# Kernel optimization log

Measured on AMD Instinct MI355X. Metric: run time of the kernel, lower is better.

The kernel has to match this reference:

```python
import jax, jax.numpy as jnp
import numpy as np

N = 50000   # nodes
E = 1600000 # edges (avg degree 32)
H = 128     # input_size == hidden_size
L = 2       # n_layer


def setup_inputs() -> dict:
    key = jax.random.key(0)
    k0, k1, k2, k3, k4 = jax.random.split(key, 5)
    inp = jax.random.normal(k0, (N, H), dtype=jnp.float32)
    h = jax.random.normal(k1, (L, N, H), dtype=jnp.float32)
    edgidx = jax.random.randint(k2, (2, E), 0, N, dtype=jnp.int32)
    # stacked gate linears, order per layer: xz, hz, xr, hr, xh, hh
    W = jax.random.normal(k3, (L, 6, H, H), dtype=jnp.float32) * (1.0 / np.sqrt(H))
    b = jax.random.normal(k4, (L, 6, H), dtype=jnp.float32) * 0.01
    return {"inp": inp, "edgidx": edgidx, "h": h, "W": W, "b": b}


def _gin(x, W, b, src, dst, n):
    # GINConv with eps=0: Linear(x + sum_{j in N(i)} x_j)
    agg = jax.ops.segment_sum(x[src], dst, num_segments=n)  # scatter-add over edges
    return (x + agg) @ W + b


def reference(inp, edgidx, h, W, b):
    src, dst = edgidx[0], edgidx[1]
    n = inp.shape[0]
    x = inp
    outs = []
    for i in range(W.shape[0]):  # small fixed layer loop
        z = jax.nn.sigmoid(_gin(x, W[i, 0], b[i, 0], src, dst, n)
                           + _gin(h[i], W[i, 1], b[i, 1], src, dst, n))
        r = jax.nn.sigmoid(_gin(x, W[i, 2], b[i, 2], src, dst, n)
                           + _gin(h[i], W[i, 3], b[i, 3], src, dst, n))
        h_tilde = jnp.tanh(_gin(x, W[i, 4], b[i, 4], src, dst, n)
                           + _gin(r * h[i], W[i, 5], b[i, 5], src, dst, n))
        x = z * h[i] + (1.0 - z) * h_tilde
        outs.append(x)
    h_out = jnp.stack(outs)  # [L, N, H]; original returns (out, h_out) where out is h_out
    return h_out
```

## Files before the change

### kernel.cpp

```cpp
#include <hip/hip_runtime.h>
#include <math.h>
#include <stdint.h>

#define HDIM 128

typedef _Float16 f16;
typedef unsigned short u16;
typedef __attribute__((ext_vector_type(8))) unsigned short u16x8;
typedef __attribute__((ext_vector_type(4))) _Float16 f16x4;
typedef __attribute__((ext_vector_type(8))) _Float16 f16x8;
typedef __attribute__((ext_vector_type(4))) float f32x4;

__global__ __launch_bounds__(256) void degrank_kernel(
    const int* __restrict__ edg, int* __restrict__ cnt,
    u16* __restrict__ rank, int E) {
  int e = blockIdx.x * 256 + threadIdx.x;
  if (e < E) {
    int src = edg[e];
    int dst = edg[E + e];
    rank[e] = (u16)atomicAdd(&cnt[dst * 16 + (src >> 12)], 1);
  }
}

__global__ __launch_bounds__(256) void nodescan_kernel(
    int* __restrict__ cnt, int* __restrict__ deg, int* __restrict__ degt,
    int N) {
  int node = blockIdx.x * 256 + threadIdx.x;
  if (node >= N) return;
  int* c = cnt + node * 16;
  int s = 0;
  #pragma unroll
  for (int b = 0; b < 16; ++b) {
    int v = c[b];
    c[b] = s;
    s += v;
  }
  degt[node] = s;
  deg[node] = (s + 7) & ~7;
}

__global__ __launch_bounds__(256) void scan_part_kernel(
    const int* __restrict__ deg, int* __restrict__ bsum, int n, int chunk) {
  __shared__ int red[256];
  const int b = blockIdx.x, t = threadIdx.x;
  const int begin = b * chunk;
  const int end = min(begin + chunk, n);
  int s = 0;
  for (int i = begin + t; i < end; i += 256) s += deg[i];
  red[t] = s;
  __syncthreads();
  for (int off = 128; off > 0; off >>= 1) {
    if (t < off) red[t] += red[t + off];
    __syncthreads();
  }
  if (t == 0) bsum[b] = red[0];
}

__global__ __launch_bounds__(256) void scan_top_kernel(
    const int* __restrict__ bsum, int* __restrict__ boff,
    int* __restrict__ offs, int n) {
  __shared__ int sh[256];
  const int t = threadIdx.x;
  int v = bsum[t];
  sh[t] = v;
  __syncthreads();
  for (int off = 1; off < 256; off <<= 1) {
    int add = (t >= off) ? sh[t - off] : 0;
    __syncthreads();
    sh[t] += add;
    __syncthreads();
  }
  boff[t] = sh[t] - v;
  if (t == 255) offs[n] = sh[255];
}

__global__ __launch_bounds__(256) void scan_fin_kernel(
    const int* __restrict__ deg, const int* __restrict__ boff,
    int* __restrict__ offs, int n, int chunk) {
  __shared__ int sh[256];
  const int b = blockIdx.x, t = threadIdx.x;
  const int idx = b * chunk + t;
  int v = (t < chunk && idx < n) ? deg[idx] : 0;
  sh[t] = v;
  __syncthreads();
  for (int off = 1; off < 256; off <<= 1) {
    int add = (t >= off) ? sh[t - off] : 0;
    __syncthreads();
    sh[t] += add;
    __syncthreads();
  }
  if (t < chunk && idx < n) offs[idx] = boff[b] + sh[t] - v;
}

__global__ __launch_bounds__(256) void fill_kernel(
    const int* __restrict__ edg, const int* __restrict__ offs,
    const int* __restrict__ cnt, const u16* __restrict__ rank,
    u16* __restrict__ csr_src, int E) {
  int i = blockIdx.x * 256 + threadIdx.x;
  int e0 = i * 4;
  if (e0 >= E) return;
  if (e0 + 4 <= E) {
    int4 s4 = *reinterpret_cast<const int4*>(edg + e0);
    int4 d4 = *reinterpret_cast<const int4*>(edg + E + e0);
    ushort4 r4 = *reinterpret_cast<const ushort4*>(rank + e0);
    csr_src[offs[d4.x] + cnt[d4.x * 16 + (s4.x >> 12)] + r4.x] = (u16)s4.x;
    csr_src[offs[d4.y] + cnt[d4.y * 16 + (s4.y >> 12)] + r4.y] = (u16)s4.y;
    csr_src[offs[d4.z] + cnt[d4.z * 16 + (s4.z >> 12)] + r4.z] = (u16)s4.z;
    csr_src[offs[d4.w] + cnt[d4.w * 16 + (s4.w >> 12)] + r4.w] = (u16)s4.w;
  } else {
    for (int e = e0; e < E; ++e) {
      int src = edg[e];
      int dst = edg[E + e];
      csr_src[offs[dst] + cnt[dst * 16 + (src >> 12)] + rank[e]] = (u16)src;
    }
  }
}

__global__ __launch_bounds__(256) void pad_kernel(
    const int* __restrict__ offs, const int* __restrict__ degt,
    const int* __restrict__ deg, u16* __restrict__ csr, int N) {
  int n = blockIdx.x * 256 + threadIdx.x;
  if (n >= N) return;
  int base = offs[n];
  int a = degt[n], b = deg[n];
  for (int k = base + a; k < base + b; ++k) csr[k] = (u16)N;
}

__global__ __launch_bounds__(256) void zpad_kernel(
    f16* __restrict__ xb, f16* __restrict__ cb, f16* __restrict__ hb,
    int N, int L) {
  int t = threadIdx.x;
  int rows = 2 + L;
  int total = 4 * rows * 4;
  if (t >= total) return;
  int chunk = t & 3;
  int r = (t >> 2) % rows;
  int sl = (t >> 2) / rows;
  size_t SN1 = (size_t)(N + 1);
  f16* p;
  if (r == 0)      p = xb + (sl * SN1 + N) * 32;
  else if (r == 1) p = cb + (sl * SN1 + N) * 32;
  else {
    int i = r - 2;
    p = hb + ((size_t)sl * L * SN1 + (size_t)i * SN1 + N) * 32;
  }
  f16x8 z{};
  *reinterpret_cast<f16x8*>(p + chunk * 8) = z;
}

__global__ __launch_bounds__(256) void convb_kernel(
    const float* __restrict__ src, f16* __restrict__ dst, int n, int SN,
    int rowoff) {
  const int t = threadIdx.x;
  const int nloc = t >> 3;
  const int sub = t & 7;
  const int sl = sub >> 1;
  const int hf = sub & 1;
  const int node = blockIdx.x * 32 + nloc;
  if (node >= n) return;
  const float* sp = src + (size_t)node * HDIM + sub * 16;
  f16* dp = dst + ((size_t)sl * SN + rowoff + node) * 32 + hf * 16;
  float4 v0 = *reinterpret_cast<const float4*>(sp + 0);
  float4 v1 = *reinterpret_cast<const float4*>(sp + 4);
  float4 v2 = *reinterpret_cast<const float4*>(sp + 8);
  float4 v3 = *reinterpret_cast<const float4*>(sp + 12);
  f16x8 o0, o1;
  o0[0]=(f16)v0.x; o0[1]=(f16)v0.y; o0[2]=(f16)v0.z; o0[3]=(f16)v0.w;
  o0[4]=(f16)v1.x; o0[5]=(f16)v1.y; o0[6]=(f16)v1.z; o0[7]=(f16)v1.w;
  o1[0]=(f16)v2.x; o1[1]=(f16)v2.y; o1[2]=(f16)v2.z; o1[3]=(f16)v2.w;
  o1[4]=(f16)v3.x; o1[5]=(f16)v3.y; o1[6]=(f16)v3.z; o1[7]=(f16)v3.w;
  *reinterpret_cast<f16x8*>(dp) = o0;
  *reinterpret_cast<f16x8*>(dp + 8) = o1;
}

__global__ __launch_bounds__(256) void transw_kernel(
    const float* __restrict__ W, f16* __restrict__ WT) {
  __shared__ float sh[32][33];
  const int g = blockIdx.y;
  const int ti = blockIdx.x >> 2;
  const int tj = blockIdx.x & 3;
  const float* __restrict__ wp = W + (size_t)g * HDIM * HDIM;
  f16* __restrict__ op = WT + (size_t)g * HDIM * HDIM;
  const int t = threadIdx.x;
  #pragma unroll
  for (int it = 0; it < 4; ++it) {
    int elem = it * 256 + t;
    int r = elem >> 5, c = elem & 31;
    sh[r][c] = wp[(size_t)(ti * 32 + r) * HDIM + tj * 32 + c];
  }
  __syncthreads();
  #pragma unroll
  for (int it = 0; it < 4; ++it) {
    int elem = it * 256 + t;
    int cc = elem >> 5, rr = elem & 31;
    op[(size_t)(tj * 32 + cc) * HDIM + ti * 32 + rr] = (f16)sh[rr][cc];
  }
}

__global__ __launch_bounds__(256) void pull2_kernel(
    const u16* __restrict__ csr_src, const int* __restrict__ offs,
    const f16* __restrict__ xb, const f16* __restrict__ hbl,
    f16* __restrict__ A, f16* __restrict__ Bh, int N, int N1, int hSN) {
  const int cls = blockIdx.x & 7;
  const int tid = cls >> 2;
  const int sl = cls & 3;
  const int node = (blockIdx.x >> 3) * 64 + (threadIdx.x >> 2);
  if (node >= N) return;
  const int c8 = (threadIdx.x & 3) << 3;
  const f16* __restrict__ tab =
      tid ? hbl + (size_t)sl * hSN * 32 : xb + (size_t)sl * (size_t)N1 * 32;
  f16* __restrict__ dst = (tid ? Bh : A) + (size_t)sl * (size_t)N1 * 32;
  const int s = offs[node];
  const int e = offs[node + 1];
  float acc[8];
  f16x8 sv = *reinterpret_cast<const f16x8*>(tab + (size_t)node * 32 + c8);
  #pragma unroll
  for (int q = 0; q < 8; ++q) acc[q] = (float)sv[q];
  int k = s;
  for (; k + 16 <= e; k += 16) {
    u16x8 ia = *reinterpret_cast<const u16x8*>(csr_src + k);
    u16x8 ib = *reinterpret_cast<const u16x8*>(csr_src + k + 8);
    f16x8 u0 = *reinterpret_cast<const f16x8*>(tab + (size_t)ia[0] * 32 + c8);
    f16x8 u1 = *reinterpret_cast<const f16x8*>(tab + (size_t)ia[1] * 32 + c8);
    f16x8 u2 = *reinterpret_cast<const f16x8*>(tab + (size_t)ia[2] * 32 + c8);
    f16x8 u3 = *reinterpret_cast<const f16x8*>(tab + (size_t)ia[3] * 32 + c8);
    f16x8 u4 = *reinterpret_cast<const f16x8*>(tab + (size_t)ia[4] * 32 + c8);
    f16x8 u5 = *reinterpret_cast<const f16x8*>(tab + (size_t)ia[5] * 32 + c8);
    f16x8 u6 = *reinterpret_cast<const f16x8*>(tab + (size_t)ia[6] * 32 + c8);
    f16x8 u7 = *reinterpret_cast<const f16x8*>(tab + (size_t)ia[7] * 32 + c8);
    f16x8 u8 = *reinterpret_cast<const f16x8*>(tab + (size_t)ib[0] * 32 + c8);
    f16x8 u9 = *reinterpret_cast<const f16x8*>(tab + (size_t)ib[1] * 32 + c8);
    f16x8 ua = *reinterpret_cast<const f16x8*>(tab + (size_t)ib[2] * 32 + c8);
    f16x8 ub = *reinterpret_cast<const f16x8*>(tab + (size_t)ib[3] * 32 + c8);
    f16x8 uc = *reinterpret_cast<const f16x8*>(tab + (size_t)ib[4] * 32 + c8);
    f16x8 ud = *reinterpret_cast<const f16x8*>(tab + (size_t)ib[5] * 32 + c8);
    f16x8 ue = *reinterpret_cast<const f16x8*>(tab + (size_t)ib[6] * 32 + c8);
    f16x8 uf = *reinterpret_cast<const f16x8*>(tab + (size_t)ib[7] * 32 + c8);
    f16x8 g0 = (u0 + u1) + (u2 + u3);
    f16x8 g1 = (u4 + u5) + (u6 + u7);
    f16x8 g2 = (u8 + u9) + (ua + ub);
    f16x8 g3 = (uc + ud) + (ue + uf);
    #pragma unroll
    for (int q = 0; q < 8; ++q)
      acc[q] += ((float)g0[q] + (float)g1[q]) + ((float)g2[q] + (float)g3[q]);
  }
  if (k < e) {
    u16x8 ia = *reinterpret_cast<const u16x8*>(csr_src + k);
    f16x8 u0 = *reinterpret_cast<const f16x8*>(tab + (size_t)ia[0] * 32 + c8);
    f16x8 u1 = *reinterpret_cast<const f16x8*>(tab + (size_t)ia[1] * 32 + c8);
    f16x8 u2 = *reinterpret_cast<const f16x8*>(tab + (size_t)ia[2] * 32 + c8);
    f16x8 u3 = *reinterpret_cast<const f16x8*>(tab + (size_t)ia[3] * 32 + c8);
    f16x8 u4 = *reinterpret_cast<const f16x8*>(tab + (size_t)ia[4] * 32 + c8);
    f16x8 u5 = *reinterpret_cast<const f16x8*>(tab + (size_t)ia[5] * 32 + c8);
    f16x8 u6 = *reinterpret_cast<const f16x8*>(tab + (size_t)ia[6] * 32 + c8);
    f16x8 u7 = *reinterpret_cast<const f16x8*>(tab + (size_t)ia[7] * 32 + c8);
    f16x8 g0 = (u0 + u1) + (u2 + u3);
    f16x8 g1 = (u4 + u5) + (u6 + u7);
    #pragma unroll
    for (int q = 0; q < 8; ++q) acc[q] += (float)g0[q] + (float)g1[q];
  }
  f16x8 o;
  #pragma unroll
  for (int q = 0; q < 8; ++q) o[q] = (f16)acc[q];
  *reinterpret_cast<f16x8*>(dst + (size_t)node * 32 + c8) = o;
}

__global__ __launch_bounds__(256) void pull1_kernel(
    const u16* __restrict__ csr_src, const int* __restrict__ offs,
    const f16* __restrict__ cb, f16* __restrict__ Ctot, int N, int N1) {
  const int sl = blockIdx.x & 3;
  const int node = (blockIdx.x >> 2) * 64 + (threadIdx.x >> 2);
  if (node >= N) return;
  const int c8 = (threadIdx.x & 3) << 3;
  const f16* __restrict__ tab = cb + (size_t)sl * (size_t)N1 * 32;
  f16* __restrict__ dst = Ctot + (size_t)sl * (size_t)N1 * 32;
  const int s = offs[node];
  const int e = offs[node + 1];
  float acc[8];
  f16x8 sv = *reinterpret_cast<const f16x8*>(tab + (size_t)node * 32 + c8);
  #pragma unroll
  for (int q = 0; q < 8; ++q) acc[q] = (float)sv[q];
  int k = s;
  for (; k + 16 <= e; k += 16) {
    u16x8 ia = *reinterpret_cast<const u16x8*>(csr_src + k);
    u16x8 ib = *reinterpret_cast<const u16x8*>(csr_src + k + 8);
    f16x8 u0 = *reinterpret_cast<const f16x8*>(tab + (size_t)ia[0] * 32 + c8);
    f16x8 u1 = *reinterpret_cast<const f16x8*>(tab + (size_t)ia[1] * 32 + c8);
    f16x8 u2 = *reinterpret_cast<const f16x8*>(tab + (size_t)ia[2] * 32 + c8);
    f16x8 u3 = *reinterpret_cast<const f16x8*>(tab + (size_t)ia[3] * 32 + c8);
    f16x8 u4 = *reinterpret_cast<const f16x8*>(tab + (size_t)ia[4] * 32 + c8);
    f16x8 u5 = *reinterpret_cast<const f16x8*>(tab + (size_t)ia[5] * 32 + c8);
    f16x8 u6 = *reinterpret_cast<const f16x8*>(tab + (size_t)ia[6] * 32 + c8);
    f16x8 u7 = *reinterpret_cast<const f16x8*>(tab + (size_t)ia[7] * 32 + c8);
    f16x8 u8 = *reinterpret_cast<const f16x8*>(tab + (size_t)ib[0] * 32 + c8);
    f16x8 u9 = *reinterpret_cast<const f16x8*>(tab + (size_t)ib[1] * 32 + c8);
    f16x8 ua = *reinterpret_cast<const f16x8*>(tab + (size_t)ib[2] * 32 + c8);
    f16x8 ub = *reinterpret_cast<const f16x8*>(tab + (size_t)ib[3] * 32 + c8);
    f16x8 uc = *reinterpret_cast<const f16x8*>(tab + (size_t)ib[4] * 32 + c8);
    f16x8 ud = *reinterpret_cast<const f16x8*>(tab + (size_t)ib[5] * 32 + c8);
    f16x8 ue = *reinterpret_cast<const f16x8*>(tab + (size_t)ib[6] * 32 + c8);
    f16x8 uf = *reinterpret_cast<const f16x8*>(tab + (size_t)ib[7] * 32 + c8);
    f16x8 g0 = (u0 + u1) + (u2 + u3);
    f16x8 g1 = (u4 + u5) + (u6 + u7);
    f16x8 g2 = (u8 + u9) + (ua + ub);
    f16x8 g3 = (uc + ud) + (ue + uf);
    #pragma unroll
    for (int q = 0; q < 8; ++q)
      acc[q] += ((float)g0[q] + (float)g1[q]) + ((float)g2[q] + (float)g3[q]);
  }
  if (k < e) {
    u16x8 ia = *reinterpret_cast<const u16x8*>(csr_src + k);
    f16x8 u0 = *reinterpret_cast<const f16x8*>(tab + (size_t)ia[0] * 32 + c8);
    f16x8 u1 = *reinterpret_cast<const f16x8*>(tab + (size_t)ia[1] * 32 + c8);
    f16x8 u2 = *reinterpret_cast<const f16x8*>(tab + (size_t)ia[2] * 32 + c8);
    f16x8 u3 = *reinterpret_cast<const f16x8*>(tab + (size_t)ia[3] * 32 + c8);
    f16x8 u4 = *reinterpret_cast<const f16x8*>(tab + (size_t)ia[4] * 32 + c8);
    f16x8 u5 = *reinterpret_cast<const f16x8*>(tab + (size_t)ia[5] * 32 + c8);
    f16x8 u6 = *reinterpret_cast<const f16x8*>(tab + (size_t)ia[6] * 32 + c8);
    f16x8 u7 = *reinterpret_cast<const f16x8*>(tab + (size_t)ia[7] * 32 + c8);
    f16x8 g0 = (u0 + u1) + (u2 + u3);
    f16x8 g1 = (u4 + u5) + (u6 + u7);
    #pragma unroll
    for (int q = 0; q < 8; ++q) acc[q] += (float)g0[q] + (float)g1[q];
  }
  f16x8 o;
  #pragma unroll
  for (int q = 0; q < 8; ++q) o[q] = (f16)acc[q];
  *reinterpret_cast<f16x8*>(dst + (size_t)node * 32 + c8) = o;
}

__device__ __forceinline__ void stage_blocked(
    const f16* __restrict__ src, f16* __restrict__ As,
    int row0, int N, int SN, int t) {
  #pragma unroll
  for (int i = 0; i < 4; ++i) {
    int u = i * 256 + t;
    int row = u >> 4;
    int sl = (u >> 2) & 3;
    int ck = u & 3;
    int r = row0 + row;
    f16x8 v{};
    if (r < N) v = *reinterpret_cast<const f16x8*>(
        src + ((size_t)sl * SN + r) * 32 + ck * 8);
    *reinterpret_cast<f16x8*>(&As[row * 136 + sl * 32 + ck * 8]) = v;
  }
}

__device__ __forceinline__ void mfma_tile(
    const f16* As, const f16* Ws, int wr, int wc, int ln15, int quad,
    f32x4 (&acc)[2][4]) {
  #pragma unroll
  for (int s = 0; s < 4; ++s) {
    f16x8 a0 = *reinterpret_cast<const f16x8*>(
        &As[(wr * 32 + ln15) * 136 + s * 32 + quad * 8]);
    f16x8 a1 = *reinterpret_cast<const f16x8*>(
        &As[(wr * 32 + 16 + ln15) * 136 + s * 32 + quad * 8]);
    #pragma unroll
    for (int ni = 0; ni < 4; ++ni) {
      f16x8 bf = *reinterpret_cast<const f16x8*>(
          &Ws[(wc * 64 + ni * 16 + ln15) * 136 + s * 32 + quad * 8]);
      acc[0][ni] = __builtin_amdgcn_mfma_f32_16x16x32_f16(a0, bf, acc[0][ni], 0, 0, 0);
      acc[1][ni] = __builtin_amdgcn_mfma_f32_16x16x32_f16(a1, bf, acc[1][ni], 0, 0, 0);
    }
  }
}

__global__ __launch_bounds__(256, 3) void gemm3_kernel(
    const f16* __restrict__ A, const f16* __restrict__ Bh,
    const f16* __restrict__ WT, const float* __restrict__ b,
    const f16* __restrict__ hbl, f16* __restrict__ zb,
    f16* __restrict__ cb, float* __restrict__ hpre, int N, int N1, int hSN) {
  __shared__ f16 As[64 * 136];
  __shared__ f16 Ws[128 * 136];
  const int t = threadIdx.x;
  const int w = t >> 6, wr = w >> 1, wc = w & 1;
  const int lane = t & 63, ln15 = lane & 15, quad = lane >> 4;
  const int row0 = blockIdx.x * 64;
  f32x4 accZ[2][4], accR[2][4], accH[2][4];
  #pragma unroll
  for (int i = 0; i < 2; ++i)
    #pragma unroll
    for (int j = 0; j < 4; ++j) {
      accZ[i][j] = (f32x4){0.f, 0.f, 0.f, 0.f};
      accR[i][j] = (f32x4){0.f, 0.f, 0.f, 0.f};
      accH[i][j] = (f32x4){0.f, 0.f, 0.f, 0.f};
    }

  stage_blocked(A, As, row0, N, N1, t);
  #pragma unroll
  for (int g = 0; g < 3; ++g) {
    const f16* __restrict__ wp = WT + (size_t)(g * 2) * HDIM * HDIM;
    __syncthreads();
    #pragma unroll
    for (int i = 0; i < 8; ++i) {
      int flat = i * 256 + t;
      int n = flat >> 4;
      int o = (flat & 15) * 8;
      *reinterpret_cast<f16x8*>(&Ws[n * 136 + o]) =
          *reinterpret_cast<const f16x8*>(wp + (size_t)n * HDIM + o);
    }
    __syncthreads();
    if (g == 0) mfma_tile(As, Ws, wr, wc, ln15, quad, accZ);
    else if (g == 1) mfma_tile(As, Ws, wr, wc, ln15, quad, accR);
    else mfma_tile(As, Ws, wr, wc, ln15, quad, accH);
  }
  __syncthreads();
  stage_blocked(Bh, As, row0, N, N1, t);
  #pragma unroll
  for (int g = 0; g < 2; ++g) {
    const f16* __restrict__ wp = WT + (size_t)(g * 2 + 1) * HDIM * HDIM;
    __syncthreads();
    #pragma unroll
    for (int i = 0; i < 8; ++i) {
      int flat = i * 256 + t;
      int n = flat >> 4;
      int o = (flat & 15) * 8;
      *reinterpret_cast<f16x8*>(&Ws[n * 136 + o]) =
          *reinterpret_cast<const f16x8*>(wp + (size_t)n * HDIM + o);
    }
    __syncthreads();
    if (g == 0) mfma_tile(As, Ws, wr, wc, ln15, quad, accZ);
    else mfma_tile(As, Ws, wr, wc, ln15, quad, accR);
  }

  #pragma unroll
  for (int ni = 0; ni < 4; ++ni) {
    const int col = wc * 64 + ni * 16 + ln15;
    const int slc = col >> 5;
    const int cw = col & 31;
    float bz = b[0 * HDIM + col] + b[1 * HDIM + col];
    float br = b[2 * HDIM + col] + b[3 * HDIM + col];
    float bh = b[4 * HDIM + col];
    #pragma unroll
    for (int mi = 0; mi < 2; ++mi) {
      #pragma unroll
      for (int r = 0; r < 4; ++r) {
        int row = row0 + wr * 32 + mi * 16 + quad * 4 + r;
        if (row >= N) continue;
        size_t idx = (size_t)row * HDIM + col;
        zb[idx] = (f16)(accZ[mi][ni][r] + bz);
        float rv = accR[mi][ni][r] + br;
        float rg = 1.f / (1.f + expf(-rv));
        float hv = (float)hbl[((size_t)slc * hSN + row) * 32 + cw];
        cb[((size_t)slc * N1 + row) * 32 + cw] = (f16)(rg * hv);
        hpre[idx] = accH[mi][ni][r] + bh;
      }
    }
  }
}

__global__ __launch_bounds__(256, 3) void gemm_final_kernel(
    const f16* __restrict__ Ctot, const f16* __restrict__ WT5,
    const float* __restrict__ b5, const f16* __restrict__ zb,
    const f16* __restrict__ hbl, float* __restrict__ outi,
    f16* __restrict__ xb, int N, int N1, int hSN) {
  __shared__ f16 As[64 * 136];
  __shared__ f16 Ws[128 * 136];
  const int t = threadIdx.x;
  const int w = t >> 6, wr = w >> 1, wc = w & 1;
  const int lane = t & 63, ln15 = lane & 15, quad = lane >> 4;
  const int row0 = blockIdx.x * 64;
  f32x4 acc[2][4];
  #pragma unroll
  for (int i = 0; i < 2; ++i)
    #pragma unroll
    for (int j = 0; j < 4; ++j) acc[i][j] = (f32x4){0.f, 0.f, 0.f, 0.f};

  stage_blocked(Ctot, As, row0, N, N1, t);
  #pragma unroll
  for (int i = 0; i < 8; ++i) {
    int flat = i * 256 + t;
    int n = flat >> 4;
    int o = (flat & 15) * 8;
    *reinterpret_cast<f16x8*>(&Ws[n * 136 + o]) =
        *reinterpret_cast<const f16x8*>(WT5 + (size_t)n * HDIM + o);
  }
  __syncthreads();
  mfma_tile(As, Ws, wr, wc, ln15, quad, acc);

  #pragma unroll
  for (int ni = 0; ni < 4; ++ni) {
    const int col = wc * 64 + ni * 16 + ln15;
    const int slc = col >> 5;
    const int cw = col & 31;
    float bias = b5[col];
    #pragma unroll
    for (int mi = 0; mi < 2; ++mi) {
      #pragma unroll
      for (int r = 0; r < 4; ++r) {
        int row = row0 + wr * 32 + mi * 16 + quad * 4 + r;
        if (row >= N) continue;
        size_t idx = (size_t)row * HDIM + col;
        float v = acc[mi][ni][r] + bias + outi[idx];
        float ht = tanhf(v);
        float z = 1.f / (1.f + expf(-(float)zb[idx]));
        float hv = (float)hbl[((size_t)slc * hSN + row) * 32 + cw];
        float o = z * hv + (1.f - z) * ht;
        outi[idx] = o;
        xb[((size_t)slc * N1 + row) * 32 + cw] = (f16)o;
      }
    }
  }
}

extern "C" void kernel_launch(void* const* d_in, const int* in_sizes, int n_in,
                              void* d_out, int out_size, void* d_ws, size_t ws_size,
                              hipStream_t stream) {
  const float* inp = (const float*)d_in[0];
  const int*   edg = (const int*)d_in[1];
  const float* h   = (const float*)d_in[2];
  const float* W   = (const float*)d_in[3];
  const float* b   = (const float*)d_in[4];
  float* out = (float*)d_out;

  const int NH = in_sizes[0];
  const int N  = NH / HDIM;
  const int E  = in_sizes[1] / 2;
  const int L  = in_sizes[2] / NH;
  const int N1 = N + 1;
  const size_t NT = (size_t)128 * N1;

  f16* Af   = (f16*)d_ws;
  f16* Bhf  = Af + NT;
  f16* cbuf = Bhf + NT;
  f16* xbuf = cbuf + NT;
  f16* hbuf = xbuf + NT;
  f16* zbuf = hbuf + (size_t)L * NT;
  f16* WT   = zbuf + (size_t)NH;
  int* deg     = (int*)(WT + (size_t)L * 6 * HDIM * HDIM);
  int* degt    = deg + N;
  int* offs    = degt + N;
  int* bsum    = offs + (N + 1);
  int* boff    = bsum + 256;
  uintptr_t rp = (uintptr_t)(boff + 256);
  rp = (rp + 63) & ~(uintptr_t)63;
  u16* rank    = (u16*)rp;
  u16* csr_src = rank + (size_t)E;
  int* cnt     = (int*)Af;

  const int eblocks = (E + 255) / 256;
  const int fblocks = (E + 1023) / 1024;
  const int nsblocks = (N + 255) / 256;
  const int rowblocks = (N + 63) / 64;
  const int p2blocks = ((N + 63) / 64) * 8;
  const int p1blocks = ((N + 63) / 64) * 4;
  const int cvblocks = (N + 31) / 32;
  const int chunk = (N + 255) / 256;
  const int hSN = L * N1;

  hipMemsetAsync(cnt, 0, (size_t)N * 16 * sizeof(int), stream);
  hipLaunchKernelGGL(degrank_kernel, dim3(eblocks), dim3(256), 0, stream,
                     edg, cnt, rank, E);
  hipLaunchKernelGGL(nodescan_kernel, dim3(nsblocks), dim3(256), 0, stream,
                     cnt, deg, degt, N);
  hipLaunchKernelGGL(scan_part_kernel, dim3(256), dim3(256), 0, stream,
                     deg, bsum, N, chunk);
  hipLaunchKernelGGL(scan_top_kernel, dim3(1), dim3(256), 0, stream,
                     bsum, boff, offs, N);
  hipLaunchKernelGGL(scan_fin_kernel, dim3(256), dim3(256), 0, stream,
                     deg, boff, offs, N, chunk);
  hipLaunchKernelGGL(fill_kernel, dim3(fblocks), dim3(256), 0, stream,
                     edg, offs, cnt, rank, csr_src, E);
  hipLaunchKernelGGL(pad_kernel, dim3(nsblocks), dim3(256), 0, stream,
                     offs, degt, deg, csr_src, N);
  hipLaunchKernelGGL(transw_kernel, dim3(16, L * 6), dim3(256), 0, stream,
                     W, WT);
  hipLaunchKernelGGL(convb_kernel, dim3(cvblocks), dim3(256), 0, stream,
                     inp, xbuf, N, N1, 0);
  for (int i = 0; i < L; ++i)
    hipLaunchKernelGGL(convb_kernel, dim3(cvblocks), dim3(256), 0, stream,
                       h + (size_t)i * NH, hbuf, N, hSN, i * N1);
  hipLaunchKernelGGL(zpad_kernel, dim3(1), dim3(256), 0, stream,
                     xbuf, cbuf, hbuf, N, L);

  for (int i = 0; i < L; ++i) {
    const f16* hbl = hbuf + (size_t)i * N1 * 32;
    const f16* WTi = WT + (size_t)i * 6 * HDIM * HDIM;
    const float* bi = b + (size_t)i * 6 * HDIM;
    float* outi = out + (size_t)i * NH;

    hipLaunchKernelGGL(pull2_kernel, dim3(p2blocks), dim3(256), 0, stream,
                       csr_src, offs, xbuf, hbl, Af, Bhf, N, N1, hSN);
    hipLaunchKernelGGL(gemm3_kernel, dim3(rowblocks), dim3(256), 0, stream,
                       Af, Bhf, WTi, bi, hbl, zbuf, cbuf, outi, N, N1, hSN);
    hipLaunchKernelGGL(pull1_kernel, dim3(p1blocks), dim3(256), 0, stream,
                       csr_src, offs, cbuf, Af, N, N1);
    hipLaunchKernelGGL(gemm_final_kernel, dim3(rowblocks), dim3(256), 0, stream,
                       Af, WTi + (size_t)5 * HDIM * HDIM, bi + 5 * HDIM,
                       zbuf, hbl, outi, xbuf, N, N1, hSN);
  }
}
```

Before: 667.2 us.

## Apply hh linear before aggregation and fuse final GRU step into pull kernel

Uses linearity of the GIN hh branch, (c + A c) W = c W + A (c W), so gemm3 now multiplies r*h by W_hh in-tile and writes the projected P. The final kernel aggregates P over neighbors and applies the tanh/GRU combine directly. This removes the separate gemm_final launch and its reload of the aggregated buffer and weights. It also merges the three conversion launches into one 2D grid and folds zero-padding into pad_kernel to cut launch count. The trade-off is extra work and shared memory traffic inside gemm3, plus aggregation of f16-rounded projected values instead of raw inputs.

```diff
diff --git a/kernel.cpp b/kernel.cpp
--- a/kernel.cpp
+++ b/kernel.cpp
@@ -118,39 +118,45 @@
 
 __global__ __launch_bounds__(256) void pad_kernel(
     const int* __restrict__ offs, const int* __restrict__ degt,
-    const int* __restrict__ deg, u16* __restrict__ csr, int N) {
+    const int* __restrict__ deg, u16* __restrict__ csr,
+    f16* __restrict__ xb, f16* __restrict__ Pb, f16* __restrict__ hb,
+    int N, int L) {
   int n = blockIdx.x * 256 + threadIdx.x;
-  if (n >= N) return;
-  int base = offs[n];
-  int a = degt[n], b = deg[n];
-  for (int k = base + a; k < base + b; ++k) csr[k] = (u16)N;
-}
-
-__global__ __launch_bounds__(256) void zpad_kernel(
-    f16* __restrict__ xb, f16* __restrict__ cb, f16* __restrict__ hb,
-    int N, int L) {
-  int t = threadIdx.x;
-  int rows = 2 + L;
-  int total = 4 * rows * 4;
-  if (t >= total) return;
-  int chunk = t & 3;
-  int r = (t >> 2) % rows;
-  int sl = (t >> 2) / rows;
-  size_t SN1 = (size_t)(N + 1);
-  f16* p;
-  if (r == 0)      p = xb + (sl * SN1 + N) * 32;
-  else if (r == 1) p = cb + (sl * SN1 + N) * 32;
-  else {
-    int i = r - 2;
-    p = hb + ((size_t)sl * L * SN1 + (size_t)i * SN1 + N) * 32;
-  }
-  f16x8 z{};
-  *reinterpret_cast<f16x8*>(p + chunk * 8) = z;
+  if (n < N) {
+    int base = offs[n];
+    int a = degt[n], b = deg[n];
+    for (int k = base + a; k < base + b; ++k) csr[k] = (u16)N;
+  } else {
+    int t2 = n - N;
+    int rows = 2 + L;
+    int total = 4 * rows * 4;
+    if (t2 < total) {
+      int chunk = t2 & 3;
+      int r = (t2 >> 2) % rows;
+      int sl = (t2 >> 2) / rows;
+      size_t SN1 = (size_t)(N + 1);
+      f16* p;
+      if (r == 0)      p = xb + (sl * SN1 + N) * 32;
+      else if (r == 1) p = Pb + (sl * SN1 + N) * 32;
+      else {
+        int i = r - 2;
+        p = hb + ((size_t)sl * L * SN1 + (size_t)i * SN1 + N) * 32;
+      }
+      f16x8 z{};
+      *reinterpret_cast<f16x8*>(p + chunk * 8) = z;
+    }
+  }
 }
 
 __global__ __launch_bounds__(256) void convb_kernel(
-    const float* __restrict__ src, f16* __restrict__ dst, int n, int SN,
-    int rowoff) {
+    const float* __restrict__ inp, const float* __restrict__ h,
+    f16* __restrict__ xb, f16* __restrict__ hb, int n, int N1, int NH,
+    int L) {
+  const int ly = blockIdx.y;
+  const float* __restrict__ src = (ly == 0) ? inp : h + (size_t)(ly - 1) * NH;
+  f16* __restrict__ dstb = (ly == 0) ? xb : hb;
+  const int SN = (ly == 0) ? N1 : L * N1;
+  const int rowoff = (ly == 0) ? 0 : (ly - 1) * N1;
   const int t = threadIdx.x;
   const int nloc = t >> 3;
   const int sub = t & 7;
@@ -159,7 +165,7 @@
   const int node = blockIdx.x * 32 + nloc;
   if (node >= n) return;
   const float* sp = src + (size_t)node * HDIM + sub * 16;
-  f16* dp = dst + ((size_t)sl * SN + rowoff + node) * 32 + hf * 16;
+  f16* dp = dstb + ((size_t)sl * SN + rowoff + node) * 32 + hf * 16;
   float4 v0 = *reinterpret_cast<const float4*>(sp + 0);
   float4 v1 = *reinterpret_cast<const float4*>(sp + 4);
   float4 v2 = *reinterpret_cast<const float4*>(sp + 8);
@@ -265,15 +271,174 @@
   *reinterpret_cast<f16x8*>(dst + (size_t)node * 32 + c8) = o;
 }
 
-__global__ __launch_bounds__(256) void pull1_kernel(
+__device__ __forceinline__ void stage_blocked(
+    const f16* __restrict__ src, f16* __restrict__ As,
+    int row0, int N, int SN, int t) {
+  #pragma unroll
+  for (int i = 0; i < 4; ++i) {
+    int u = i * 256 + t;
+    int row = u >> 4;
+    int sl = (u >> 2) & 3;
+    int ck = u & 3;
+    int r = row0 + row;
+    f16x8 v{};
+    if (r < N) v = *reinterpret_cast<const f16x8*>(
+        src + ((size_t)sl * SN + r) * 32 + ck * 8);
+    *reinterpret_cast<f16x8*>(&As[row * 136 + sl * 32 + ck * 8]) = v;
+  }
+}
+
+__device__ __forceinline__ void mfma_tile(
+    const f16* As, const f16* Ws, int wr, int wc, int ln15, int quad,
+    f32x4 (&acc)[2][4]) {
+  #pragma unroll
+  for (int s = 0; s < 4; ++s) {
+    f16x8 a0 = *reinterpret_cast<const f16x8*>(
+        &As[(wr * 32 + ln15) * 136 + s * 32 + quad * 8]);
+    f16x8 a1 = *reinterpret_cast<const f16x8*>(
+        &As[(wr * 32 + 16 + ln15) * 136 + s * 32 + quad * 8]);
+    #pragma unroll
+    for (int ni = 0; ni < 4; ++ni) {
+      f16x8 bf = *reinterpret_cast<const f16x8*>(
+          &Ws[(wc * 64 + ni * 16 + ln15) * 136 + s * 32 + quad * 8]);
+      acc[0][ni] = __builtin_amdgcn_mfma_f32_16x16x32_f16(a0, bf, acc[0][ni], 0, 0, 0);
+      acc[1][ni] = __builtin_amdgcn_mfma_f32_16x16x32_f16(a1, bf, acc[1][ni], 0, 0, 0);
+    }
+  }
+}
+
+__global__ __launch_bounds__(256, 3) void gemm3_kernel(
+    const f16* __restrict__ A, const f16* __restrict__ Bh,
+    const f16* __restrict__ WT, const float* __restrict__ b,
+    const f16* __restrict__ hbl, f16* __restrict__ zb,
+    f16* __restrict__ P, float* __restrict__ hpre, int N, int N1, int hSN) {
+  __shared__ f16 As[64 * 136];
+  __shared__ f16 Ws[128 * 136];
+  const int t = threadIdx.x;
+  const int w = t >> 6, wr = w >> 1, wc = w & 1;
+  const int lane = t & 63, ln15 = lane & 15, quad = lane >> 4;
+  const int row0 = blockIdx.x * 64;
+  f32x4 accZ[2][4], accR[2][4], accH[2][4];
+  #pragma unroll
+  for (int i = 0; i < 2; ++i)
+    #pragma unroll
+    for (int j = 0; j < 4; ++j) {
+      accZ[i][j] = (f32x4){0.f, 0.f, 0.f, 0.f};
+      accR[i][j] = (f32x4){0.f, 0.f, 0.f, 0.f};
+      accH[i][j] = (f32x4){0.f, 0.f, 0.f, 0.f};
+    }
+
+  stage_blocked(A, As, row0, N, N1, t);
+  #pragma unroll
+  for (int g = 0; g < 3; ++g) {
+    const f16* __restrict__ wp = WT + (size_t)(g * 2) * HDIM * HDIM;
+    __syncthreads();
+    #pragma unroll
+    for (int i = 0; i < 8; ++i) {
+      int flat = i * 256 + t;
+      int n = flat >> 4;
+      int o = (flat & 15) * 8;
+      *reinterpret_cast<f16x8*>(&Ws[n * 136 + o]) =
+          *reinterpret_cast<const f16x8*>(wp + (size_t)n * HDIM + o);
+    }
+    __syncthreads();
+    if (g == 0) mfma_tile(As, Ws, wr, wc, ln15, quad, accZ);
+    else if (g == 1) mfma_tile(As, Ws, wr, wc, ln15, quad, accR);
+    else mfma_tile(As, Ws, wr, wc, ln15, quad, accH);
+  }
+  __syncthreads();
+  stage_blocked(Bh, As, row0, N, N1, t);
+  #pragma unroll
+  for (int g = 0; g < 2; ++g) {
+    const f16* __restrict__ wp = WT + (size_t)(g * 2 + 1) * HDIM * HDIM;
+    __syncthreads();
+    #pragma unroll
+    for (int i = 0; i < 8; ++i) {
+      int flat = i * 256 + t;
+      int n = flat >> 4;
+      int o = (flat & 15) * 8;
+      *reinterpret_cast<f16x8*>(&Ws[n * 136 + o]) =
+          *reinterpret_cast<const f16x8*>(wp + (size_t)n * HDIM + o);
+    }
+    __syncthreads();
+    if (g == 0) mfma_tile(As, Ws, wr, wc, ln15, quad, accZ);
+    else mfma_tile(As, Ws, wr, wc, ln15, quad, accR);
+  }
+  __syncthreads();
+
+  {
+    const f16* __restrict__ wp = WT + (size_t)5 * HDIM * HDIM;
+    #pragma unroll
+    for (int i = 0; i < 8; ++i) {
+      int flat = i * 256 + t;
+      int n = flat >> 4;
+      int o = (flat & 15) * 8;
+      *reinterpret_cast<f16x8*>(&Ws[n * 136 + o]) =
+          *reinterpret_cast<const f16x8*>(wp + (size_t)n * HDIM + o);
+    }
+  }
+  #pragma unroll
+  for (int ni = 0; ni < 4; ++ni) {
+    const int col = wc * 64 + ni * 16 + ln15;
+    const int slc = col >> 5;
+    const int cw = col & 31;
+    float bz = b[0 * HDIM + col] + b[1 * HDIM + col];
+    float br = b[2 * HDIM + col] + b[3 * HDIM + col];
+    float bh = b[4 * HDIM + col] + b[5 * HDIM + col];
+    #pragma unroll
+    for (int mi = 0; mi < 2; ++mi) {
+      #pragma unroll
+      for (int r = 0; r < 4; ++r) {
+        int rowl = wr * 32 + mi * 16 + quad * 4 + r;
+        int row = row0 + rowl;
+        float rv = accR[mi][ni][r] + br;
+        float rg = 1.f / (1.f + expf(-rv));
+        float hv = 0.f;
+        if (row < N) {
+          size_t idx = (size_t)row * HDIM + col;
+          zb[idx] = (f16)(accZ[mi][ni][r] + bz);
+          hpre[idx] = accH[mi][ni][r] + bh;
+          hv = (float)hbl[((size_t)slc * hSN + row) * 32 + cw];
+        }
+        As[rowl * 136 + col] = (f16)(rg * hv);
+      }
+    }
+  }
+  __syncthreads();
+  f32x4 accP[2][4];
+  #pragma unroll
+  for (int i = 0; i < 2; ++i)
+    #pragma unroll
+    for (int j = 0; j < 4; ++j) accP[i][j] = (f32x4){0.f, 0.f, 0.f, 0.f};
+  mfma_tile(As, Ws, wr, wc, ln15, quad, accP);
+
+  #pragma unroll
+  for (int ni = 0; ni < 4; ++ni) {
+    const int col = wc * 64 + ni * 16 + ln15;
+    const int slc = col >> 5;
+    const int cw = col & 31;
+    #pragma unroll
+    for (int mi = 0; mi < 2; ++mi) {
+      #pragma unroll
+      for (int r = 0; r < 4; ++r) {
+        int row = row0 + wr * 32 + mi * 16 + quad * 4 + r;
+        if (row >= N) continue;
+        P[((size_t)slc * N1 + row) * 32 + cw] = (f16)accP[mi][ni][r];
+      }
+    }
+  }
+}
+
+__global__ __launch_bounds__(256) void gru_final_kernel(
     const u16* __restrict__ csr_src, const int* __restrict__ offs,
-    const f16* __restrict__ cb, f16* __restrict__ Ctot, int N, int N1) {
+    const f16* __restrict__ P, const f16* __restrict__ zb,
+    const f16* __restrict__ hbl, float* __restrict__ outi,
+    f16* __restrict__ xb, int N, int N1, int hSN) {
   const int sl = blockIdx.x & 3;
   const int node = (blockIdx.x >> 2) * 64 + (threadIdx.x >> 2);
   if (node >= N) return;
   const int c8 = (threadIdx.x & 3) << 3;
-  const f16* __restrict__ tab = cb + (size_t)sl * (size_t)N1 * 32;
-  f16* __restrict__ dst = Ctot + (size_t)sl * (size_t)N1 * 32;
+  const f16* __restrict__ tab = P + (size_t)sl * (size_t)N1 * 32;
   const int s = offs[node];
   const int e = offs[node + 1];
   float acc[8];
@@ -323,184 +488,26 @@
     #pragma unroll
     for (int q = 0; q < 8; ++q) acc[q] += (float)g0[q] + (float)g1[q];
   }
-  f16x8 o;
-  #pragma unroll
-  for (int q = 0; q < 8; ++q) o[q] = (f16)acc[q];
-  *reinterpret_cast<f16x8*>(dst + (size_t)node * 32 + c8) = o;
-}
-
-__device__ __forceinline__ void stage_blocked(
-    const f16* __restrict__ src, f16* __restrict__ As,
-    int row0, int N, int SN, int t) {
-  #pragma unroll
-  for (int i = 0; i < 4; ++i) {
-    int u = i * 256 + t;
-    int row = u >> 4;
-    int sl = (u >> 2) & 3;
-    int ck = u & 3;
-    int r = row0 + row;
-    f16x8 v{};
-    if (r < N) v = *reinterpret_cast<const f16x8*>(
-        src + ((size_t)sl * SN + r) * 32 + ck * 8);
-    *reinterpret_cast<f16x8*>(&As[row * 136 + sl * 32 + ck * 8]) = v;
-  }
-}
-
-__device__ __forceinline__ void mfma_tile(
-    const f16* As, const f16* Ws, int wr, int wc, int ln15, int quad,
-    f32x4 (&acc)[2][4]) {
-  #pragma unroll
-  for (int s = 0; s < 4; ++s) {
-    f16x8 a0 = *reinterpret_cast<const f16x8*>(
-        &As[(wr * 32 + ln15) * 136 + s * 32 + quad * 8]);
-    f16x8 a1 = *reinterpret_cast<const f16x8*>(
-        &As[(wr * 32 + 16 + ln15) * 136 + s * 32 + quad * 8]);
-    #pragma unroll
-    for (int ni = 0; ni < 4; ++ni) {
-      f16x8 bf = *reinterpret_cast<const f16x8*>(
-          &Ws[(wc * 64 + ni * 16 + ln15) * 136 + s * 32 + quad * 8]);
-      acc[0][ni] = __builtin_amdgcn_mfma_f32_16x16x32_f16(a0, bf, acc[0][ni], 0, 0, 0);
-      acc[1][ni] = __builtin_amdgcn_mfma_f32_16x16x32_f16(a1, bf, acc[1][ni], 0, 0, 0);
-    }
-  }
-}
-
-__global__ __launch_bounds__(256, 3) void gemm3_kernel(
-    const f16* __restrict__ A, const f16* __restrict__ Bh,
-    const f16* __restrict__ WT, const float* __restrict__ b,
-    const f16* __restrict__ hbl, f16* __restrict__ zb,
-    f16* __restrict__ cb, float* __restrict__ hpre, int N, int N1, int hSN) {
-  __shared__ f16 As[64 * 136];
-  __shared__ f16 Ws[128 * 136];
-  const int t = threadIdx.x;
-  const int w = t >> 6, wr = w >> 1, wc = w & 1;
-  const int lane = t & 63, ln15 = lane & 15, quad = lane >> 4;
-  const int row0 = blockIdx.x * 64;
-  f32x4 accZ[2][4], accR[2][4], accH[2][4];
-  #pragma unroll
-  for (int i = 0; i < 2; ++i)
-    #pragma unroll
-    for (int j = 0; j < 4; ++j) {
-      accZ[i][j] = (f32x4){0.f, 0.f, 0.f, 0.f};
-      accR[i][j] = (f32x4){0.f, 0.f, 0.f, 0.f};
-      accH[i][j] = (f32x4){0.f, 0.f, 0.f, 0.f};
-    }
-
-  stage_blocked(A, As, row0, N, N1, t);
-  #pragma unroll
-  for (int g = 0; g < 3; ++g) {
-    const f16* __restrict__ wp = WT + (size_t)(g * 2) * HDIM * HDIM;
-    __syncthreads();
-    #pragma unroll
-    for (int i = 0; i < 8; ++i) {
-      int flat = i * 256 + t;
-      int n = flat >> 4;
-      int o = (flat & 15) * 8;
-      *reinterpret_cast<f16x8*>(&Ws[n * 136 + o]) =
-          *reinterpret_cast<const f16x8*>(wp + (size_t)n * HDIM + o);
-    }
-    __syncthreads();
-    if (g == 0) mfma_tile(As, Ws, wr, wc, ln15, quad, accZ);
-    else if (g == 1) mfma_tile(As, Ws, wr, wc, ln15, quad, accR);
-    else mfma_tile(As, Ws, wr, wc, ln15, quad, accH);
-  }
-  __syncthreads();
-  stage_blocked(Bh, As, row0, N, N1, t);
-  #pragma unroll
-  for (int g = 0; g < 2; ++g) {
-    const f16* __restrict__ wp = WT + (size_t)(g * 2 + 1) * HDIM * HDIM;
-    __syncthreads();
-    #pragma unroll
-    for (int i = 0; i < 8; ++i) {
-      int flat = i * 256 + t;
-      int n = flat >> 4;
-      int o = (flat & 15) * 8;
-      *reinterpret_cast<f16x8*>(&Ws[n * 136 + o]) =
-          *reinterpret_cast<const f16x8*>(wp + (size_t)n * HDIM + o);
-    }
-    __syncthreads();
-    if (g == 0) mfma_tile(As, Ws, wr, wc, ln15, quad, accZ);
-    else mfma_tile(As, Ws, wr, wc, ln15, quad, accR);
-  }
-
-  #pragma unroll
-  for (int ni = 0; ni < 4; ++ni) {
-    const int col = wc * 64 + ni * 16 + ln15;
-    const int slc = col >> 5;
-    const int cw = col & 31;
-    float bz = b[0 * HDIM + col] + b[1 * HDIM + col];
-    float br = b[2 * HDIM + col] + b[3 * HDIM + col];
-    float bh = b[4 * HDIM + col];
-    #pragma unroll
-    for (int mi = 0; mi < 2; ++mi) {
-      #pragma unroll
-      for (int r = 0; r < 4; ++r) {
-        int row = row0 + wr * 32 + mi * 16 + quad * 4 + r;
-        if (row >= N) continue;
-        size_t idx = (size_t)row * HDIM + col;
-        zb[idx] = (f16)(accZ[mi][ni][r] + bz);
-        float rv = accR[mi][ni][r] + br;
-        float rg = 1.f / (1.f + expf(-rv));
-        float hv = (float)hbl[((size_t)slc * hSN + row) * 32 + cw];
-        cb[((size_t)slc * N1 + row) * 32 + cw] = (f16)(rg * hv);
-        hpre[idx] = accH[mi][ni][r] + bh;
-      }
-    }
-  }
-}
-
-__global__ __launch_bounds__(256, 3) void gemm_final_kernel(
-    const f16* __restrict__ Ctot, const f16* __restrict__ WT5,
-    const float* __restrict__ b5, const f16* __restrict__ zb,
-    const f16* __restrict__ hbl, float* __restrict__ outi,
-    f16* __restrict__ xb, int N, int N1, int hSN) {
-  __shared__ f16 As[64 * 136];
-  __shared__ f16 Ws[128 * 136];
-  const int t = threadIdx.x;
-  const int w = t >> 6, wr = w >> 1, wc = w & 1;
-  const int lane = t & 63, ln15 = lane & 15, quad = lane >> 4;
-  const int row0 = blockIdx.x * 64;
-  f32x4 acc[2][4];
-  #pragma unroll
-  for (int i = 0; i < 2; ++i)
-    #pragma unroll
-    for (int j = 0; j < 4; ++j) acc[i][j] = (f32x4){0.f, 0.f, 0.f, 0.f};
-
-  stage_blocked(Ctot, As, row0, N, N1, t);
-  #pragma unroll
-  for (int i = 0; i < 8; ++i) {
-    int flat = i * 256 + t;
-    int n = flat >> 4;
-    int o = (flat & 15) * 8;
-    *reinterpret_cast<f16x8*>(&Ws[n * 136 + o]) =
-        *reinterpret_cast<const f16x8*>(WT5 + (size_t)n * HDIM + o);
-  }
-  __syncthreads();
-  mfma_tile(As, Ws, wr, wc, ln15, quad, acc);
-
-  #pragma unroll
-  for (int ni = 0; ni < 4; ++ni) {
-    const int col = wc * 64 + ni * 16 + ln15;
-    const int slc = col >> 5;
-    const int cw = col & 31;
-    float bias = b5[col];
-    #pragma unroll
-    for (int mi = 0; mi < 2; ++mi) {
-      #pragma unroll
-      for (int r = 0; r < 4; ++r) {
-        int row = row0 + wr * 32 + mi * 16 + quad * 4 + r;
-        if (row >= N) continue;
-        size_t idx = (size_t)row * HDIM + col;
-        float v = acc[mi][ni][r] + bias + outi[idx];
-        float ht = tanhf(v);
-        float z = 1.f / (1.f + expf(-(float)zb[idx]));
-        float hv = (float)hbl[((size_t)slc * hSN + row) * 32 + cw];
-        float o = z * hv + (1.f - z) * ht;
-        outi[idx] = o;
-        xb[((size_t)slc * N1 + row) * 32 + cw] = (f16)o;
-      }
-    }
-  }
+  const size_t idx = (size_t)node * HDIM + sl * 32 + c8;
+  float4 hp0 = *reinterpret_cast<const float4*>(outi + idx);
+  float4 hp1 = *reinterpret_cast<const float4*>(outi + idx + 4);
+  f16x8 zv = *reinterpret_cast<const f16x8*>(zb + idx);
+  f16x8 hv = *reinterpret_cast<const f16x8*>(
+      hbl + ((size_t)sl * hSN + node) * 32 + c8);
+  float4 o0, o1;
+  f16x8 xo;
+  #pragma unroll
+  for (int q = 0; q < 8; ++q) {
+    float hp = (q < 4) ? (&hp0.x)[q] : (&hp1.x)[q - 4];
+    float ht = tanhf(hp + acc[q]);
+    float z = 1.f / (1.f + expf(-(float)zv[q]));
+    float o = z * (float)hv[q] + (1.f - z) * ht;
+    if (q < 4) (&o0.x)[q] = o; else (&o1.x)[q - 4] = o;
+    xo[q] = (f16)o;
+  }
+  *reinterpret_cast<float4*>(outi + idx) = o0;
+  *reinterpret_cast<float4*>(outi + idx + 4) = o1;
+  *reinterpret_cast<f16x8*>(xb + ((size_t)sl * N1 + node) * 32 + c8) = xo;
 }
 
 extern "C" void kernel_launch(void* const* d_in, const int* in_sizes, int n_in,
@@ -522,8 +529,8 @@
 
   f16* Af   = (f16*)d_ws;
   f16* Bhf  = Af + NT;
-  f16* cbuf = Bhf + NT;
-  f16* xbuf = cbuf + NT;
+  f16* Pbuf = Bhf + NT;
+  f16* xbuf = Pbuf + NT;
   f16* hbuf = xbuf + NT;
   f16* zbuf = hbuf + (size_t)L * NT;
   f16* WT   = zbuf + (size_t)NH;
@@ -541,6 +548,7 @@
   const int eblocks = (E + 255) / 256;
   const int fblocks = (E + 1023) / 1024;
   const int nsblocks = (N + 255) / 256;
+  const int pdblocks = (N + 256 + 255) / 256;
   const int rowblocks = (N + 63) / 64;
   const int p2blocks = ((N + 63) / 64) * 8;
   const int p1blocks = ((N + 63) / 64) * 4;
@@ -561,17 +569,12 @@
                      deg, boff, offs, N, chunk);
   hipLaunchKernelGGL(fill_kernel, dim3(fblocks), dim3(256), 0, stream,
                      edg, offs, cnt, rank, csr_src, E);
-  hipLaunchKernelGGL(pad_kernel, dim3(nsblocks), dim3(256), 0, stream,
-                     offs, degt, deg, csr_src, N);
+  hipLaunchKernelGGL(pad_kernel, dim3(pdblocks), dim3(256), 0, stream,
+                     offs, degt, deg, csr_src, xbuf, Pbuf, hbuf, N, L);
   hipLaunchKernelGGL(transw_kernel, dim3(16, L * 6), dim3(256), 0, stream,
                      W, WT);
-  hipLaunchKernelGGL(convb_kernel, dim3(cvblocks), dim3(256), 0, stream,
-                     inp, xbuf, N, N1, 0);
-  for (int i = 0; i < L; ++i)
-    hipLaunchKernelGGL(convb_kernel, dim3(cvblocks), dim3(256), 0, stream,
-                       h + (size_t)i * NH, hbuf, N, hSN, i * N1);
-  hipLaunchKernelGGL(zpad_kernel, dim3(1), dim3(256), 0, stream,
-                     xbuf, cbuf, hbuf, N, L);
+  hipLaunchKernelGGL(convb_kernel, dim3(cvblocks, L + 1), dim3(256), 0, stream,
+                     inp, h, xbuf, hbuf, N, N1, NH, L);
 
   for (int i = 0; i < L; ++i) {
     const f16* hbl = hbuf + (size_t)i * N1 * 32;
@@ -582,11 +585,8 @@
     hipLaunchKernelGGL(pull2_kernel, dim3(p2blocks), dim3(256), 0, stream,
                        csr_src, offs, xbuf, hbl, Af, Bhf, N, N1, hSN);
     hipLaunchKernelGGL(gemm3_kernel, dim3(rowblocks), dim3(256), 0, stream,
-                       Af, Bhf, WTi, bi, hbl, zbuf, cbuf, outi, N, N1, hSN);
-    hipLaunchKernelGGL(pull1_kernel, dim3(p1blocks), dim3(256), 0, stream,
-                       csr_src, offs, cbuf, Af, N, N1);
-    hipLaunchKernelGGL(gemm_final_kernel, dim3(rowblocks), dim3(256), 0, stream,
-                       Af, WTi + (size_t)5 * HDIM * HDIM, bi + 5 * HDIM,
-                       zbuf, hbl, outi, xbuf, N, N1, hSN);
-  }
-}
+                       Af, Bhf, WTi, bi, hbl, zbuf, Pbuf, outi, N, N1, hSN);
+    hipLaunchKernelGGL(gru_final_kernel, dim3(p1blocks), dim3(256), 0, stream,
+                       csr_src, offs, Pbuf, zbuf, hbl, outi, xbuf, N, N1, hSN);
+  }
+}
```

Measured after the change: 591.7 us. 11.3% less time.
